# Optimization experiments

Hardware: AMD Instinct MI355X
Metric: run time of the kernel (lower is better)

The kernel has to match this reference:

```python
import jax, jax.numpy as jnp
import numpy as np

EPS = 1e-8
LAMBDA_SOFTMAX = 9.0
LAMBDA_LSE = 6.0
LEAKY = 0.1


def _l2norm(x, axis):
    n = jnp.sqrt(jnp.sum(x * x, axis=axis, keepdims=True)) + EPS
    return x / n


def setup_inputs() -> dict:
    key = jax.random.key(0)
    k1, k2, k3, k4 = jax.random.split(key, 4)
    n_img, n_cap, n_region, max_w, img_dim, d = 64, 64, 36, 32, 2048, 1024
    images = jax.random.normal(k1, (n_img, n_region, img_dim), dtype=jnp.float32)
    cap_emb = jax.random.normal(k2, (n_cap, max_w, d), dtype=jnp.float32)
    # Xavier-uniform fc like EncoderImagePrecomp.init_weights
    r = np.sqrt(6.0) / np.sqrt(img_dim + d)
    W_fc = jax.random.uniform(k3, (img_dim, d), dtype=jnp.float32, minval=-r, maxval=r)
    b_fc = jnp.zeros((d,), dtype=jnp.float32)
    cap_lens = jnp.maximum(jax.random.randint(k4, (n_cap,), 0, max_w), 4).astype(jnp.int32)
    return {"images": images, "cap_emb": cap_emb, "W_fc": W_fc, "b_fc": b_fc, "cap_lens": cap_lens}


def reference(images, cap_emb, W_fc, b_fc, cap_lens):
    # EncoderImagePrecomp: linear projection + l2norm over feature dim
    img_emb = _l2norm(images @ W_fc + b_fc, axis=-1)          # (I, R, d)
    # text_norm (EncoderText applies l2norm to cap_emb)
    cap = _l2norm(cap_emb, axis=-1)                           # (C, W, d)

    C, W = cap.shape[0], cap.shape[1]
    mask = (jnp.arange(W)[None, :] < cap_lens[:, None]).astype(cap.dtype)  # (C, W)

    # func_attention (t2i): query=caption words, context=image regions
    # attn = bmm(context, query^T): (C, I, R, W)
    attn = jnp.einsum('ird,cwd->cirw', img_emb, cap)
    # clipped_l2norm: LeakyReLU(0.1) then l2norm over the word (queryL) axis,
    # with padded words zeroed so the norm matches the ragged per-caption slice
    attn = jnp.where(attn > 0, attn, LEAKY * attn)
    attn = attn * mask[:, None, None, :]
    attn = _l2norm(attn, axis=-1)
    # transpose -> (C, I, W, R), temperature softmax over regions
    attn = jnp.swapaxes(attn, 2, 3)
    attn = jax.nn.softmax(attn * LAMBDA_SOFTMAX, axis=-1)     # (C, I, W, R)
    # weightedContext = attn @ images: (C, I, W, d)
    wctx = jnp.einsum('ciwr,ird->ciwd', attn, img_emb)

    # cosine similarity between caption words and weighted context
    w12 = jnp.einsum('cwd,ciwd->ciw', cap, wctx)
    w1 = jnp.sqrt(jnp.sum(cap * cap, axis=-1))[:, None, :]     # (C, 1, W)
    w2 = jnp.sqrt(jnp.sum(wctx * wctx, axis=-1))               # (C, I, W)
    row_sim = w12 / jnp.maximum(w1 * w2, EPS)                  # (C, I, W)

    # LogSumExp aggregation over valid words only
    e = jnp.exp(row_sim * LAMBDA_LSE) * mask[:, None, :]
    sim = jnp.log(jnp.sum(e, axis=-1)) / LAMBDA_LSE            # (C, I)
    # torch code concatenates per-caption columns -> (n_image, n_caption)
    return sim.T
```

## Files before the change

kernel.cpp:

```cpp
#include <hip/hip_runtime.h>

constexpr int NI = 64;
constexpr int NC = 64;
constexpr int RR = 36;
constexpr int WW = 32;
constexpr int DI = 2048;
constexpr int DD = 1024;
constexpr int MROWS = NI * RR;
constexpr int NCOLS = NC * WW;

#define EPSV 1e-8f
#define LAM_SM 9.0f
#define LAM_LSE 6.0f
#define LEAKY_S 0.1f

typedef __bf16 bf16x8 __attribute__((ext_vector_type(8)));
typedef float f32x4 __attribute__((ext_vector_type(4)));
typedef unsigned short ushort8v __attribute__((ext_vector_type(8)));
typedef unsigned short ushort4v __attribute__((ext_vector_type(4)));

__device__ __forceinline__ unsigned short f2bf(float f) {
    unsigned int u = __builtin_bit_cast(unsigned int, f);
    unsigned int r = (u + 0x7fffu + ((u >> 16) & 1u)) >> 16;
    return (unsigned short)r;
}

#define GLOAD16(gp, lp)                                                              \
    __builtin_amdgcn_global_load_lds(                                                \
        (const __attribute__((address_space(1))) unsigned int*)(gp),                 \
        (__attribute__((address_space(3))) unsigned int*)(lp), 16, 0, 0)

__global__ __launch_bounds__(256) void prep(const float* __restrict__ images,
                                            const float* __restrict__ W,
                                            const float* __restrict__ cap,
                                            unsigned short* __restrict__ images_bf,
                                            unsigned short* __restrict__ Wt,
                                            unsigned short* __restrict__ capn_bf,
                                            float* __restrict__ w1)
{
    const int b = blockIdx.x, tid = threadIdx.x;
    if (b < 2304) {
        int i = b * 256 + tid;
        const float4* X4 = reinterpret_cast<const float4*>(images);
        float4 a = X4[i * 2], c = X4[i * 2 + 1];
        ushort8v o;
        o[0] = f2bf(a.x); o[1] = f2bf(a.y); o[2] = f2bf(a.z); o[3] = f2bf(a.w);
        o[4] = f2bf(c.x); o[5] = f2bf(c.y); o[6] = f2bf(c.z); o[7] = f2bf(c.w);
        *reinterpret_cast<ushort8v*>(&images_bf[i * 8]) = o;
    } else if (b < 4352) {
        __shared__ float t[32][33];
        int bi = b - 2304;
        int bk = (bi >> 5) * 32;
        int bn = (bi & 31) * 32;
        int x = tid & 31, y0 = tid >> 5;
        for (int yy = y0; yy < 32; yy += 8)
            t[yy][x] = W[(bk + yy) * DD + bn + x];
        __syncthreads();
        for (int yy = y0; yy < 32; yy += 8)
            Wt[(bn + yy) * DI + bk + x] = f2bf(t[x][yy]);
    } else {
        int row = b - 4352;
        float4 v = *reinterpret_cast<const float4*>(&cap[row * 1024 + tid * 4]);
        float s = v.x * v.x + v.y * v.y + v.z * v.z + v.w * v.w;
        #pragma unroll
        for (int off = 32; off; off >>= 1) s += __shfl_down(s, off);
        __shared__ float ps[4];
        if ((tid & 63) == 0) ps[tid >> 6] = s;
        __syncthreads();
        float tot = ps[0] + ps[1] + ps[2] + ps[3];
        float n = sqrtf(tot);
        float inv = 1.0f / (n + EPSV);
        v.x *= inv; v.y *= inv; v.z *= inv; v.w *= inv;
        ushort4v o;
        o[0] = f2bf(v.x); o[1] = f2bf(v.y); o[2] = f2bf(v.z); o[3] = f2bf(v.w);
        *reinterpret_cast<ushort4v*>(&capn_bf[row * 1024 + tid * 4]) = o;
        if (tid == 0) w1[row] = n * inv;
    }
}

template <int M, int N, int K, int KS>
__global__ __launch_bounds__(256) void gemm_proj64(const unsigned short* __restrict__ A,
                                                   const unsigned short* __restrict__ Bt,
                                                   float* __restrict__ C)
{
    __shared__ __align__(16) unsigned short As[64 * 64];
    __shared__ __align__(16) unsigned short Bs[128 * 64];
    const int tid = threadIdx.x;
    const int w = tid >> 6, lane = tid & 63;
    const int bm = blockIdx.x * 64, bn = blockIdx.y * 128;
    const int klo = blockIdx.z * (K / KS);
    const int wr = w >> 1, wc = w & 1;
    const int hi = lane >> 4, fr = lane & 15;

    f32x4 acc[2][4] = {};

    const unsigned short* gA[2];
    const unsigned short* gB[4];
    unsigned short* lA[2];
    unsigned short* lB[4];
    #pragma unroll
    for (int n = 0; n < 2; ++n) {
        int s = tid + n * 256;
        int row = s >> 3, j = (s & 7) ^ (row & 7);
        gA[n] = &A[(size_t)(bm + row) * K + klo + j * 8];
        lA[n] = &As[s * 8];
    }
    #pragma unroll
    for (int n = 0; n < 4; ++n) {
        int s = tid + n * 256;
        int row = s >> 3, j = (s & 7) ^ (row & 7);
        gB[n] = &Bt[(size_t)(bn + row) * K + klo + j * 8];
        lB[n] = &Bs[s * 8];
    }

    for (int k0 = 0; k0 < K / KS; k0 += 64) {
        __syncthreads();
        #pragma unroll
        for (int n = 0; n < 2; ++n) GLOAD16(gA[n] + k0, lA[n]);
        #pragma unroll
        for (int n = 0; n < 4; ++n) GLOAD16(gB[n] + k0, lB[n]);
        __syncthreads();
        #pragma unroll
        for (int ks = 0; ks < 2; ++ks) {
            bf16x8 af[2], bfv[4];
            #pragma unroll
            for (int mi = 0; mi < 2; ++mi) {
                int row = wr * 32 + mi * 16 + fr;
                af[mi] = *reinterpret_cast<const bf16x8*>(
                    &As[row * 64 + ((((ks << 2) + hi) ^ (row & 7)) << 3)]);
            }
            #pragma unroll
            for (int ni = 0; ni < 4; ++ni) {
                int row = wc * 64 + ni * 16 + fr;
                bfv[ni] = *reinterpret_cast<const bf16x8*>(
                    &Bs[row * 64 + ((((ks << 2) + hi) ^ (row & 7)) << 3)]);
            }
            #pragma unroll
            for (int mi = 0; mi < 2; ++mi)
                #pragma unroll
                for (int ni = 0; ni < 4; ++ni)
                    acc[mi][ni] = __builtin_amdgcn_mfma_f32_16x16x32_bf16(af[mi], bfv[ni], acc[mi][ni], 0, 0, 0);
        }
    }

    float* Cz = C + (size_t)blockIdx.z * M * N;
    const int cr0 = hi * 4, cc = fr;
    #pragma unroll
    for (int mi = 0; mi < 2; ++mi) {
        int row0 = bm + wr * 32 + mi * 16 + cr0;
        #pragma unroll
        for (int ni = 0; ni < 4; ++ni) {
            int col = bn + wc * 64 + ni * 16 + cc;
            #pragma unroll
            for (int r = 0; r < 4; ++r)
                Cz[(size_t)(row0 + r) * N + col] = acc[mi][ni][r];
        }
    }
}

__global__ __launch_bounds__(256) void rownorm_add(float* __restrict__ P0,
                                                   const float* __restrict__ P1,
                                                   const float* __restrict__ bias,
                                                   unsigned short* __restrict__ Xbf)
{
    const int row = blockIdx.x;
    const int t4 = threadIdx.x * 4;
    float4 a = *reinterpret_cast<float4*>(&P0[row * 1024 + t4]);
    float4 b = *reinterpret_cast<const float4*>(&P1[row * 1024 + t4]);
    float4 c = *reinterpret_cast<const float4*>(&bias[t4]);
    float4 v = {a.x + b.x + c.x, a.y + b.y + c.y, a.z + b.z + c.z, a.w + b.w + c.w};
    float s = v.x * v.x + v.y * v.y + v.z * v.z + v.w * v.w;
    #pragma unroll
    for (int off = 32; off; off >>= 1) s += __shfl_down(s, off);
    __shared__ float ps[4];
    if ((threadIdx.x & 63) == 0) ps[threadIdx.x >> 6] = s;
    __syncthreads();
    float tot = ps[0] + ps[1] + ps[2] + ps[3];
    float inv = 1.0f / (sqrtf(tot) + EPSV);
    v.x *= inv; v.y *= inv; v.z *= inv; v.w *= inv;
    *reinterpret_cast<float4*>(&P0[row * 1024 + t4]) = v;
    ushort4v o;
    o[0] = f2bf(v.x); o[1] = f2bf(v.y); o[2] = f2bf(v.z); o[3] = f2bf(v.w);
    *reinterpret_cast<ushort4v*>(&Xbf[row * 1024 + t4]) = o;
}

__global__ __launch_bounds__(128) void gram_rows(const float* __restrict__ emb,
                                                 unsigned short* __restrict__ G_bf)
{
    const int b = blockIdx.x;
    const int i = b / RR, r = b % RR;
    const int wv = threadIdx.x >> 6;
    const int lane = threadIdx.x & 63;
    if (threadIdx.x < 28) G_bf[(size_t)(i * RR + r) * 64 + 36 + threadIdx.x] = 0;
    float a[16];
    const float* rowp = &emb[(i * RR + r) * DD + lane * 16];
    #pragma unroll
    for (int q = 0; q < 4; ++q) {
        float4 v = *reinterpret_cast<const float4*>(&rowp[q * 4]);
        a[q * 4 + 0] = v.x; a[q * 4 + 1] = v.y; a[q * 4 + 2] = v.z; a[q * 4 + 3] = v.w;
    }
    for (int rp = r + wv; rp < RR; rp += 2) {
        const float* bp = &emb[(i * RR + rp) * DD + lane * 16];
        float s = 0.f;
        #pragma unroll
        for (int q = 0; q < 4; ++q) {
            float4 v = *reinterpret_cast<const float4*>(&bp[q * 4]);
            s += a[q * 4 + 0] * v.x + a[q * 4 + 1] * v.y + a[q * 4 + 2] * v.z + a[q * 4 + 3] * v.w;
        }
        #pragma unroll
        for (int off = 32; off; off >>= 1) s += __shfl_xor(s, off);
        if (lane == 0) {
            unsigned short sb = f2bf(s);
            G_bf[(size_t)(i * RR + r) * 64 + rp] = sb;
            G_bf[(size_t)(i * RR + rp) * 64 + r] = sb;
        }
    }
}

__global__ __launch_bounds__(256) void sim_fused(const unsigned short* __restrict__ img_bf,
                                                 const unsigned short* __restrict__ capn_bf,
                                                 const unsigned short* __restrict__ G_bf,
                                                 const float* __restrict__ w1v,
                                                 const int* __restrict__ cap_lens,
                                                 float* __restrict__ out)
{
    __shared__ __align__(16) unsigned short As[48 * 32];
    __shared__ __align__(16) unsigned short Bs[128 * 32];
    __shared__ __align__(16) unsigned short Gb[48 * 64];
    __shared__ __align__(16) unsigned short Eb[4][32 * 64];
    const int tid = threadIdx.x;
    const int w = tid >> 6, lane = tid & 63;
    const int i = blockIdx.y, cg = blockIdx.x;
    const int c = cg * 4 + w;
    const int hi = lane >> 4, lo = lane & 15;

    {
        const unsigned int* gsrc = (const unsigned int*)(G_bf + (size_t)i * RR * 64);
        unsigned int* gdst = (unsigned int*)Gb;
        for (int e = tid; e < 36 * 32; e += 256) gdst[e] = gsrc[e];
        for (int e = tid; e < 12 * 32; e += 256) gdst[36 * 32 + e] = 0;
        unsigned int* ed = (unsigned int*)Eb;
        for (int e2 = tid; e2 < 4 * 32 * 8; e2 += 256) {
            int slab = e2 >> 8, rem = e2 & 255;
            int row = rem >> 3, q = rem & 7;
            ed[slab * 1024 + row * 32 + 24 + q] = 0;
        }
    }

    f32x4 acc[3][2] = {};
    const unsigned short* gA0 = &img_bf[(size_t)(i * RR + (tid >> 2)) * DD + (tid & 3) * 8];
    const unsigned short* gB0 = &capn_bf[(size_t)(cg * 128 + (tid >> 2)) * DD + (tid & 3) * 8];
    unsigned short* lA0 = &As[w * 512];
    unsigned short* lB0 = &Bs[w * 512];
    const int kgrp = hi * 8;

    for (int k0 = 0; k0 < DD; k0 += 32) {
        __syncthreads();
        if (w < 3) GLOAD16(gA0 + k0, lA0);
        GLOAD16(gB0 + k0, lB0);
        GLOAD16(gB0 + 64 * DD + k0, lB0 + 2048);
        __syncthreads();
        bf16x8 b0 = *reinterpret_cast<const bf16x8*>(&Bs[(w * 32 + lo) * 32 + kgrp]);
        bf16x8 b1 = *reinterpret_cast<const bf16x8*>(&Bs[(w * 32 + 16 + lo) * 32 + kgrp]);
        #pragma unroll
        for (int mi = 0; mi < 3; ++mi) {
            bf16x8 af = *reinterpret_cast<const bf16x8*>(&As[(mi * 16 + lo) * 32 + kgrp]);
            acc[mi][0] = __builtin_amdgcn_mfma_f32_16x16x32_bf16(af, b0, acc[mi][0], 0, 0, 0);
            acc[mi][1] = __builtin_amdgcn_mfma_f32_16x16x32_bf16(af, b1, acc[mi][1], 0, 0, 0);
        }
    }

    const int len = cap_lens[c];

    float a1[3][2][4];
    #pragma unroll
    for (int mi = 0; mi < 3; ++mi)
        #pragma unroll
        for (int reg = 0; reg < 4; ++reg) {
            int r = mi * 16 + hi * 4 + reg;
            float v0 = acc[mi][0][reg]; v0 = v0 > 0.f ? v0 : LEAKY_S * v0; v0 = (lo < len) ? v0 : 0.f;
            float v1 = acc[mi][1][reg]; v1 = v1 > 0.f ? v1 : LEAKY_S * v1; v1 = (16 + lo < len) ? v1 : 0.f;
            float ss = v0 * v0 + v1 * v1;
            ss += __shfl_xor(ss, 1); ss += __shfl_xor(ss, 2);
            ss += __shfl_xor(ss, 4); ss += __shfl_xor(ss, 8);
            float inv = 1.0f / (sqrtf(ss) + EPSV);
            bool valid = r < RR;
            a1[mi][0][reg] = valid ? v0 * inv : -1e30f;
            a1[mi][1][reg] = valid ? v1 * inv : -1e30f;
        }

    float m0 = -1e30f, m1 = -1e30f;
    #pragma unroll
    for (int mi = 0; mi < 3; ++mi)
        #pragma unroll
        for (int reg = 0; reg < 4; ++reg) {
            m0 = fmaxf(m0, a1[mi][0][reg]);
            m1 = fmaxf(m1, a1[mi][1][reg]);
        }
    m0 = fmaxf(m0, __shfl_xor(m0, 16)); m0 = fmaxf(m0, __shfl_xor(m0, 32));
    m1 = fmaxf(m1, __shfl_xor(m1, 16)); m1 = fmaxf(m1, __shfl_xor(m1, 32));

    float e_[3][2][4];
    float w12p0 = 0.f, w12p1 = 0.f;
    #pragma unroll
    for (int mi = 0; mi < 3; ++mi)
        #pragma unroll
        for (int reg = 0; reg < 4; ++reg) {
            int r = mi * 16 + hi * 4 + reg;
            bool valid = r < RR;
            float e0 = valid ? __expf(LAM_SM * (a1[mi][0][reg] - m0)) : 0.f;
            float e1 = valid ? __expf(LAM_SM * (a1[mi][1][reg] - m1)) : 0.f;
            e_[mi][0][reg] = e0; e_[mi][1][reg] = e1;
            w12p0 += e0 * acc[mi][0][reg];
            w12p1 += e1 * acc[mi][1][reg];
            Eb[w][(lo) * 64 + r] = f2bf(e0);
            Eb[w][(16 + lo) * 64 + r] = f2bf(e1);
        }
    w12p0 += __shfl_xor(w12p0, 16); w12p0 += __shfl_xor(w12p0, 32);
    w12p1 += __shfl_xor(w12p1, 16); w12p1 += __shfl_xor(w12p1, 32);
    __syncthreads();

    f32x4 T[3][2] = {};
    #pragma unroll
    for (int kk = 0; kk < 2; ++kk) {
        int kg2 = kk * 32 + hi * 8;
        bf16x8 eb0 = *reinterpret_cast<const bf16x8*>(&Eb[w][(lo) * 64 + kg2]);
        bf16x8 eb1 = *reinterpret_cast<const bf16x8*>(&Eb[w][(16 + lo) * 64 + kg2]);
        #pragma unroll
        for (int mi = 0; mi < 3; ++mi) {
            bf16x8 gf = *reinterpret_cast<const bf16x8*>(&Gb[(mi * 16 + lo) * 64 + kg2]);
            T[mi][0] = __builtin_amdgcn_mfma_f32_16x16x32_bf16(gf, eb0, T[mi][0], 0, 0, 0);
            T[mi][1] = __builtin_amdgcn_mfma_f32_16x16x32_bf16(gf, eb1, T[mi][1], 0, 0, 0);
        }
    }
    float w20 = 0.f, w21 = 0.f;
    #pragma unroll
    for (int mi = 0; mi < 3; ++mi)
        #pragma unroll
        for (int reg = 0; reg < 4; ++reg) {
            w20 += e_[mi][0][reg] * T[mi][0][reg];
            w21 += e_[mi][1][reg] * T[mi][1][reg];
        }
    w20 += __shfl_xor(w20, 16); w20 += __shfl_xor(w20, 32);
    w21 += __shfl_xor(w21, 16); w21 += __shfl_xor(w21, 32);

    float ew = 0.f;
    if (lo < len) {
        float rs = w12p0 / fmaxf(w1v[c * WW + lo] * sqrtf(fmaxf(w20, 0.f)), 1e-30f);
        ew += __expf(LAM_LSE * rs);
    }
    if (16 + lo < len) {
        float rs = w12p1 / fmaxf(w1v[c * WW + 16 + lo] * sqrtf(fmaxf(w21, 0.f)), 1e-30f);
        ew += __expf(LAM_LSE * rs);
    }
    ew += __shfl_xor(ew, 1); ew += __shfl_xor(ew, 2);
    ew += __shfl_xor(ew, 4); ew += __shfl_xor(ew, 8);
    if (lane == 0) out[i * NC + c] = logf(ew) / LAM_LSE;
}

extern "C" void kernel_launch(void* const* d_in, const int* in_sizes, int n_in,
                              void* d_out, int out_size, void* d_ws, size_t ws_size,
                              hipStream_t stream)
{
    const float* images   = (const float*)d_in[0];
    const float* cap_emb  = (const float*)d_in[1];
    const float* W_fc     = (const float*)d_in[2];
    const float* b_fc     = (const float*)d_in[3];
    const int*   cap_lens = (const int*)d_in[4];
    float* out = (float*)d_out;

    char* ws = (char*)d_ws;
    float*          part0     = (float*)(ws);
    float*          part1     = (float*)(ws + 9437184);
    unsigned short* images_bf = (unsigned short*)(ws + 18874368);
    unsigned short* Wt        = (unsigned short*)(ws + 28311552);
    unsigned short* img_bf    = (unsigned short*)(ws + 32505856);
    unsigned short* capn_bf   = (unsigned short*)(ws + 37224448);
    unsigned short* G_bf      = (unsigned short*)(ws + 41418752);
    float*          w1        = (float*)(ws + 41713664);

    prep<<<6400, 256, 0, stream>>>(images, W_fc, cap_emb, images_bf, Wt, capn_bf, w1);
    gemm_proj64<MROWS, DD, DI, 2><<<dim3(MROWS / 64, DD / 128, 2), 256, 0, stream>>>(images_bf, Wt, part0);
    rownorm_add<<<MROWS, 256, 0, stream>>>(part0, part1, b_fc, img_bf);
    gram_rows<<<MROWS, 128, 0, stream>>>(part0, G_bf);
    sim_fused<<<dim3(16, NI), 256, 0, stream>>>(img_bf, capn_bf, G_bf, w1, cap_lens, out);
}
```

Baseline: 165.4 us.

## Compute region Gram matrix inside sim_fused via MFMA instead of separate kernel

```diff
diff --git a/kernel.cpp b/kernel.cpp
--- a/kernel.cpp
+++ b/kernel.cpp
@@ -158,14 +158,14 @@
     }
 }
 
-__global__ __launch_bounds__(256) void rownorm_add(float* __restrict__ P0,
+__global__ __launch_bounds__(256) void rownorm_add(const float* __restrict__ P0,
                                                    const float* __restrict__ P1,
                                                    const float* __restrict__ bias,
                                                    unsigned short* __restrict__ Xbf)
 {
     const int row = blockIdx.x;
     const int t4 = threadIdx.x * 4;
-    float4 a = *reinterpret_cast<float4*>(&P0[row * 1024 + t4]);
+    float4 a = *reinterpret_cast<const float4*>(&P0[row * 1024 + t4]);
     float4 b = *reinterpret_cast<const float4*>(&P1[row * 1024 + t4]);
     float4 c = *reinterpret_cast<const float4*>(&bias[t4]);
     float4 v = {a.x + b.x + c.x, a.y + b.y + c.y, a.z + b.z + c.z, a.w + b.w + c.w};
@@ -178,48 +178,13 @@
     float tot = ps[0] + ps[1] + ps[2] + ps[3];
     float inv = 1.0f / (sqrtf(tot) + EPSV);
     v.x *= inv; v.y *= inv; v.z *= inv; v.w *= inv;
-    *reinterpret_cast<float4*>(&P0[row * 1024 + t4]) = v;
     ushort4v o;
     o[0] = f2bf(v.x); o[1] = f2bf(v.y); o[2] = f2bf(v.z); o[3] = f2bf(v.w);
     *reinterpret_cast<ushort4v*>(&Xbf[row * 1024 + t4]) = o;
 }
 
-__global__ __launch_bounds__(128) void gram_rows(const float* __restrict__ emb,
-                                                 unsigned short* __restrict__ G_bf)
-{
-    const int b = blockIdx.x;
-    const int i = b / RR, r = b % RR;
-    const int wv = threadIdx.x >> 6;
-    const int lane = threadIdx.x & 63;
-    if (threadIdx.x < 28) G_bf[(size_t)(i * RR + r) * 64 + 36 + threadIdx.x] = 0;
-    float a[16];
-    const float* rowp = &emb[(i * RR + r) * DD + lane * 16];
-    #pragma unroll
-    for (int q = 0; q < 4; ++q) {
-        float4 v = *reinterpret_cast<const float4*>(&rowp[q * 4]);
-        a[q * 4 + 0] = v.x; a[q * 4 + 1] = v.y; a[q * 4 + 2] = v.z; a[q * 4 + 3] = v.w;
-    }
-    for (int rp = r + wv; rp < RR; rp += 2) {
-        const float* bp = &emb[(i * RR + rp) * DD + lane * 16];
-        float s = 0.f;
-        #pragma unroll
-        for (int q = 0; q < 4; ++q) {
-            float4 v = *reinterpret_cast<const float4*>(&bp[q * 4]);
-            s += a[q * 4 + 0] * v.x + a[q * 4 + 1] * v.y + a[q * 4 + 2] * v.z + a[q * 4 + 3] * v.w;
-        }
-        #pragma unroll
-        for (int off = 32; off; off >>= 1) s += __shfl_xor(s, off);
-        if (lane == 0) {
-            unsigned short sb = f2bf(s);
-            G_bf[(size_t)(i * RR + r) * 64 + rp] = sb;
-            G_bf[(size_t)(i * RR + rp) * 64 + r] = sb;
-        }
-    }
-}
-
 __global__ __launch_bounds__(256) void sim_fused(const unsigned short* __restrict__ img_bf,
                                                  const unsigned short* __restrict__ capn_bf,
-                                                 const unsigned short* __restrict__ G_bf,
                                                  const float* __restrict__ w1v,
                                                  const int* __restrict__ cap_lens,
                                                  float* __restrict__ out)
@@ -235,19 +200,18 @@
     const int hi = lane >> 4, lo = lane & 15;
 
     {
-        const unsigned int* gsrc = (const unsigned int*)(G_bf + (size_t)i * RR * 64);
         unsigned int* gdst = (unsigned int*)Gb;
-        for (int e = tid; e < 36 * 32; e += 256) gdst[e] = gsrc[e];
-        for (int e = tid; e < 12 * 32; e += 256) gdst[36 * 32 + e] = 0;
+        for (int e = tid; e < 48 * 8; e += 256)
+            gdst[(e >> 3) * 32 + 24 + (e & 7)] = 0;
         unsigned int* ed = (unsigned int*)Eb;
         for (int e2 = tid; e2 < 4 * 32 * 8; e2 += 256) {
             int slab = e2 >> 8, rem = e2 & 255;
-            int row = rem >> 3, q = rem & 7;
-            ed[slab * 1024 + row * 32 + 24 + q] = 0;
+            ed[slab * 1024 + (rem >> 3) * 32 + 24 + (rem & 7)] = 0;
         }
     }
 
     f32x4 acc[3][2] = {};
+    f32x4 gacc[3] = {};
     const unsigned short* gA0 = &img_bf[(size_t)(i * RR + (tid >> 2)) * DD + (tid & 3) * 8];
     const unsigned short* gB0 = &capn_bf[(size_t)(cg * 128 + (tid >> 2)) * DD + (tid & 3) * 8];
     unsigned short* lA0 = &As[w * 512];
@@ -262,12 +226,28 @@
         __syncthreads();
         bf16x8 b0 = *reinterpret_cast<const bf16x8*>(&Bs[(w * 32 + lo) * 32 + kgrp]);
         bf16x8 b1 = *reinterpret_cast<const bf16x8*>(&Bs[(w * 32 + 16 + lo) * 32 + kgrp]);
+        bf16x8 af[3];
+        #pragma unroll
+        for (int mi = 0; mi < 3; ++mi)
+            af[mi] = *reinterpret_cast<const bf16x8*>(&As[(mi * 16 + lo) * 32 + kgrp]);
         #pragma unroll
         for (int mi = 0; mi < 3; ++mi) {
-            bf16x8 af = *reinterpret_cast<const bf16x8*>(&As[(mi * 16 + lo) * 32 + kgrp]);
-            acc[mi][0] = __builtin_amdgcn_mfma_f32_16x16x32_bf16(af, b0, acc[mi][0], 0, 0, 0);
-            acc[mi][1] = __builtin_amdgcn_mfma_f32_16x16x32_bf16(af, b1, acc[mi][1], 0, 0, 0);
-        }
+            acc[mi][0] = __builtin_amdgcn_mfma_f32_16x16x32_bf16(af[mi], b0, acc[mi][0], 0, 0, 0);
+            acc[mi][1] = __builtin_amdgcn_mfma_f32_16x16x32_bf16(af[mi], b1, acc[mi][1], 0, 0, 0);
+        }
+        if (w < 3) {
+            #pragma unroll
+            for (int j = 0; j < 3; ++j)
+                gacc[j] = __builtin_amdgcn_mfma_f32_16x16x32_bf16(af[w], af[j], gacc[j], 0, 0, 0);
+        }
+    }
+
+    if (w < 3) {
+        #pragma unroll
+        for (int j = 0; j < 3; ++j)
+            #pragma unroll
+            for (int reg = 0; reg < 4; ++reg)
+                Gb[(w * 16 + hi * 4 + reg) * 64 + j * 16 + lo] = f2bf(gacc[j][reg]);
     }
 
     const int len = cap_lens[c];
@@ -376,12 +356,10 @@
     unsigned short* Wt        = (unsigned short*)(ws + 28311552);
     unsigned short* img_bf    = (unsigned short*)(ws + 32505856);
     unsigned short* capn_bf   = (unsigned short*)(ws + 37224448);
-    unsigned short* G_bf      = (unsigned short*)(ws + 41418752);
     float*          w1        = (float*)(ws + 41713664);
 
     prep<<<6400, 256, 0, stream>>>(images, W_fc, cap_emb, images_bf, Wt, capn_bf, w1);
     gemm_proj64<MROWS, DD, DI, 2><<<dim3(MROWS / 64, DD / 128, 2), 256, 0, stream>>>(images_bf, Wt, part0);
     rownorm_add<<<MROWS, 256, 0, stream>>>(part0, part1, b_fc, img_bf);
-    gram_rows<<<MROWS, 128, 0, stream>>>(part0, G_bf);
-    sim_fused<<<dim3(16, NI), 256, 0, stream>>>(img_bf, capn_bf, G_bf, w1, cap_lens, out);
-}
+    sim_fused<<<dim3(16, NI), 256, 0, stream>>>(img_bf, capn_bf, w1, cap_lens, out);
+}
```

After: 231.5 us. +40.0%, slower.
